# Performance work log

Hardware: AMD Instinct MI355X
Metric: run time of the kernel (lower is better)

The kernel has to match this reference:

```python
import jax, jax.numpy as jnp
import numpy as np

N_HEAD = 16
N_KV_HEAD = 4
D_HEAD = 128
RMS_EPS = 1.1920929e-07  # torch default eps for fp32 rms_norm


def _rms_norm(x):
    return x * jax.lax.rsqrt(jnp.mean(x * x, axis=-1, keepdims=True) + RMS_EPS)


def _rotary_tables(n_pos, dim):
    # dim = d_head; freq table has dim//2 entries (half of them zero)
    angular_freq = (1.0 / 1024.0) ** jnp.linspace(0.0, 1.0, dim // 4, dtype=jnp.float32)
    angular_freq = jnp.concatenate([angular_freq, jnp.zeros(dim // 4, jnp.float32)])
    theta = jnp.arange(n_pos, dtype=jnp.float32)[:, None] * angular_freq[None, :]
    return jnp.cos(theta), jnp.sin(theta)


def _apply_rotary(x):
    # x: (B, H, T, D). Faithful to source: cos/sin indexed by x.shape[-3] (= H),
    # broadcast over the time axis.
    n = x.shape[-3]
    cos, sin = _rotary_tables(n, x.shape[-1])
    cos = cos[None, :, None, :]
    sin = sin[None, :, None, :]
    xf = x.astype(jnp.float32)
    x1, x2 = jnp.split(xf, 2, axis=-1)
    y1 = x1 * cos + x2 * sin
    y2 = -x1 * sin + x2 * cos
    return jnp.concatenate([y1, y2], axis=-1).astype(x.dtype)


def setup_inputs() -> dict:
    key = jax.random.key(0)
    k1, k2, k3, k4 = jax.random.split(key, 4)
    B, T, C = 2, 2048, 2048
    return {
        "x": jax.random.normal(k1, (B, T, C), jnp.float32),
        "Wq": jax.random.normal(k2, (C, C), jnp.float32) * 0.02,
        "Wkv": jax.random.normal(k3, (2 * N_KV_HEAD * D_HEAD, C), jnp.float32) * 0.02,
        "Wproj": jax.random.normal(k4, (C, C), jnp.float32) * 0.02,
        "tok_masks": jnp.ones((B, T), jnp.int32),
    }


def reference(x, Wq, Wkv, Wproj, tok_masks):
    B, T, C = x.shape
    nh, nkv, dh = N_HEAD, N_KV_HEAD, D_HEAD

    q = (x @ Wq.T).reshape(B, T, nh, dh).transpose(0, 2, 1, 3)          # (B,nh,T,dh)
    kv = x @ Wkv.T                                                       # (B,T,2*nkv*dh)
    k, v = jnp.split(kv, 2, axis=2)
    k = k.reshape(B, T, nkv, dh).transpose(0, 2, 1, 3)                   # (B,nkv,T,dh)
    v = v.reshape(B, T, nkv, dh).transpose(0, 2, 1, 3)

    q, k = _rms_norm(q), _rms_norm(k)
    q, k = _apply_rotary(q), _apply_rotary(k)

    # GQA: repeat kv heads to match query heads
    rep = nh // nkv
    k = jnp.repeat(k, rep, axis=1)
    v = jnp.repeat(v, rep, axis=1)

    scale = 1.0 / jnp.sqrt(jnp.float32(dh))
    scores = jnp.einsum("bhqd,bhkd->bhqk", q, k) * scale                 # (B,nh,T,T)
    causal = jnp.tril(jnp.ones((T, T), bool))
    scores = jnp.where(causal[None, None], scores, -jnp.inf)
    attn = jax.nn.softmax(scores, axis=-1)
    y = jnp.einsum("bhqk,bhkd->bhqd", attn, v)                           # (B,nh,T,dh)
    y = y.transpose(0, 2, 1, 3).reshape(B, T, C)
    y = y @ Wproj.T
    return (y, jnp.float32(0.0))
```

## Files before the change

kernel.cpp:

```cpp
#include <hip/hip_runtime.h>
#include <hip/hip_bf16.h>

#define T_SEQ 2048
#define BATCH 2
#define CDIM  2048
#define NH    16
#define NKV   4
#define DH    128

typedef __attribute__((ext_vector_type(8))) short bfrag;
typedef __attribute__((ext_vector_type(4))) float ffrag;
typedef __hip_bfloat16 bf16;

#if defined(__has_builtin)
#if __has_builtin(__builtin_amdgcn_global_load_lds)
#define USE_GLL 1
#endif
#endif
#ifndef USE_GLL
#define USE_GLL 0
#endif

__device__ __forceinline__ void stage16(const bf16* __restrict__ g, bf16* lds_base, int lane) {
#if USE_GLL
    __builtin_amdgcn_global_load_lds((const __attribute__((address_space(1))) void*)g,
                                     (__attribute__((address_space(3))) void*)lds_base, 16, 0, 0);
#else
    *(bfrag*)(lds_base + lane * 8) = *(const bfrag*)g;
#endif
}

struct bf16x4 { bf16 a, b, c, d; };
#define N4_X   (BATCH * T_SEQ * CDIM / 4)
#define N4_WQ  (CDIM * CDIM / 4)
#define N4_WKV (2 * NKV * DH * CDIM / 4)
#define N4_WP  (CDIM * CDIM / 4)
__global__ __launch_bounds__(256) void cast_all(
    const float* __restrict__ x, const float* __restrict__ wq,
    const float* __restrict__ wkv, const float* __restrict__ wp,
    bf16* __restrict__ xb, bf16* __restrict__ wqb, bf16* __restrict__ wkvb, bf16* __restrict__ wpb)
{
    int j = blockIdx.x * 256 + threadIdx.x;
    const float* s; bf16* d;
    if (j < N4_X) { s = x; d = xb; }
    else {
        j -= N4_X;
        if (j < N4_WQ) { s = wq; d = wqb; }
        else {
            j -= N4_WQ;
            if (j < N4_WKV) { s = wkv; d = wkvb; }
            else { j -= N4_WKV; if (j >= N4_WP) return; s = wp; d = wpb; }
        }
    }
    float4 f = ((const float4*)s)[j];
    bf16x4 o{__float2bfloat16(f.x), __float2bfloat16(f.y),
             __float2bfloat16(f.z), __float2bfloat16(f.w)};
    ((bf16x4*)d)[j] = o;
}

template<int MODE>
__device__ __forceinline__ void gemm_body(
    const bf16* __restrict__ A, const bf16* __restrict__ W, int m0, int n0,
    bf16* __restrict__ out0, bf16* __restrict__ out1, float* __restrict__ outf)
{
    __shared__ __align__(16) bf16 sA[128 * 32];
    __shared__ __align__(16) bf16 sB[128 * 32];
    const int lane = threadIdx.x & 63;
    const int w = threadIdx.x >> 6;
    const int lr = lane & 15, quad = lane >> 4;
    const int m_off = (w & 1) * 64, n_off = (w >> 1) * 64;

    const int srow = lane >> 2;
    const int ssw  = (srow + (srow >> 2)) & 3;
    const bf16* ap = A + (size_t)(m0 + w * 32 + srow) * CDIM + (((lane & 3) ^ ssw)) * 8;
    const bf16* bp = W + (size_t)(n0 + w * 32 + srow) * CDIM + (((lane & 3) ^ ssw)) * 8;
    bf16* sA0 = &sA[(w * 32) * 32];
    bf16* sA1 = &sA[(w * 32 + 16) * 32];
    bf16* sB0 = &sB[(w * 32) * 32];
    bf16* sB1 = &sB[(w * 32 + 16) * 32];

    const int rsw = (lr + (lr >> 2)) & 3;
    const int ccol = ((quad ^ rsw)) * 8;

    ffrag acc[4][4] = {};
    for (int kk = 0; kk < CDIM; kk += 32) {
        __syncthreads();
        stage16(ap, sA0, lane);
        stage16(ap + (size_t)16 * CDIM, sA1, lane);
        stage16(bp, sB0, lane);
        stage16(bp + (size_t)16 * CDIM, sB1, lane);
        ap += 32; bp += 32;
        __syncthreads();

        bfrag af[4], bg[4];
        #pragma unroll
        for (int s = 0; s < 4; ++s) af[s] = *(const bfrag*)&sA[(m_off + s * 16 + lr) * 32 + ccol];
        #pragma unroll
        for (int s = 0; s < 4; ++s) bg[s] = *(const bfrag*)&sB[(n_off + s * 16 + lr) * 32 + ccol];
        #pragma unroll
        for (int i = 0; i < 4; ++i)
            #pragma unroll
            for (int j = 0; j < 4; ++j)
                acc[i][j] = __builtin_amdgcn_mfma_f32_16x16x32_bf16(af[i], bg[j], acc[i][j], 0, 0, 0);
    }

    #pragma unroll
    for (int si = 0; si < 4; ++si) {
        #pragma unroll
        for (int sj = 0; sj < 4; ++sj) {
            #pragma unroll
            for (int i = 0; i < 4; ++i) {
                int m = m0 + m_off + si * 16 + quad * 4 + i;
                int n = n0 + n_off + sj * 16 + lr;
                float v = acc[si][sj][i];
                if (MODE == 0) {
                    int b = m >> 11, t = m & (T_SEQ - 1);
                    int h = n >> 7, d = n & (DH - 1);
                    out0[(((size_t)(b * NH + h) * T_SEQ + t) << 7) + d] = __float2bfloat16(v);
                } else if (MODE == 1) {
                    int b = m >> 11, t = m & (T_SEQ - 1);
                    if (n < NKV * DH) {
                        int h = n >> 7, d = n & (DH - 1);
                        out0[(((size_t)(b * NKV + h) * T_SEQ + t) << 7) + d] = __float2bfloat16(v);
                    } else {
                        int n2 = n - NKV * DH;
                        int h = n2 >> 7, d = n2 & (DH - 1);
                        out1[(((size_t)(b * NKV + h) * DH + d) << 11) + t] = __float2bfloat16(v);
                    }
                } else {
                    outf[(size_t)m * CDIM + n] = v;
                }
            }
        }
    }
}

__global__ __launch_bounds__(256) void gemm_qkv(
    const bf16* __restrict__ A, const bf16* __restrict__ Wq, const bf16* __restrict__ Wkv,
    bf16* __restrict__ q, bf16* __restrict__ k, bf16* __restrict__ vt)
{
    if (blockIdx.y < 16)
        gemm_body<0>(A, Wq, blockIdx.x * 128, blockIdx.y * 128, q, nullptr, nullptr);
    else
        gemm_body<1>(A, Wkv, blockIdx.x * 128, (blockIdx.y - 16) * 128, k, vt, nullptr);
}

__global__ __launch_bounds__(256) void gemm_proj(
    const bf16* __restrict__ A, const bf16* __restrict__ W, float* __restrict__ outf)
{
    gemm_body<2>(A, W, blockIdx.x * 128, blockIdx.y * 128, nullptr, nullptr, outf);
    if (blockIdx.x == 0 && blockIdx.y == 0 && threadIdx.x == 0)
        outf[(size_t)BATCH * T_SEQ * CDIM] = 0.0f;
}

#define QROWS (BATCH * NH * T_SEQ)
#define KROWS (BATCH * NKV * T_SEQ)
__global__ __launch_bounds__(256) void normrope_k(bf16* __restrict__ qb, bf16* __restrict__ kb) {
    int row = blockIdx.x * 4 + (threadIdx.x >> 6);
    bf16* bufb; int nheads;
    if (row < QROWS) { bufb = qb; nheads = NH; }
    else { row -= QROWS; bufb = kb; nheads = NKV; }
    const int h = (row >> 11) % nheads;
    bf16* p = bufb + (size_t)row * DH;
    const int d = threadIdx.x & 63;
    float x1 = __bfloat162float(p[d]);
    float x2 = __bfloat162float(p[d + 64]);
    float ss = x1 * x1 + x2 * x2;
    #pragma unroll
    for (int off = 32; off; off >>= 1) ss += __shfl_xor(ss, off);
    float r = rsqrtf(ss * (1.0f / 128.0f) + 1.1920929e-07f);
    x1 *= r; x2 *= r;
    float freq = (d < 32) ? exp2f(-10.0f * (float)d * (1.0f / 31.0f)) : 0.0f;
    float th = (float)h * freq;
    float c, s;
    __sincosf(th, &s, &c);
    p[d]      = __float2bfloat16(x1 * c + x2 * s);
    p[d + 64] = __float2bfloat16(-x1 * s + x2 * c);
}

__global__ __launch_bounds__(512, 2) void attn_k(const bf16* __restrict__ Q, const bf16* __restrict__ K,
                                                 const bf16* __restrict__ VT, bf16* __restrict__ Y)
{
    const int lane = threadIdx.x & 63;
    const int w = threadIdx.x >> 6;
    const int g = w >> 2, wl = w & 3;
    const int p = blockIdx.x, h = blockIdx.y, b = blockIdx.z;
    const int lr = lane & 15, quad = lane >> 4, lk = quad * 8;
    const bf16* Qb = Q  + (size_t)(b * NH  + h)        * T_SEQ * DH;
    const bf16* Kb = K  + (size_t)(b * NKV + (h >> 2)) * T_SEQ * DH;
    const bf16* Vb = VT + (size_t)(b * NKV + (h >> 2)) * DH * T_SEQ;

    __shared__ __align__(16) union ShmU {
        struct { bf16 SK[2][32 * 128]; bf16 SV[2][128 * 32]; bf16 SP[8][2][16 * 32]; } s;
        ffrag MRG[9 * 4 * 64];
    } shm;
    bf16* SKg = shm.s.SK[g];
    bf16* SVg = shm.s.SV[g];

    const int k_r0 = wl * 8 + (lane >> 4);
    const int k_ch = lane & 15;
    const int v_r0 = wl * 32 + (lane >> 2);
    const int v_ch = lane & 3;
    const int vsw = (lr + (lr >> 2)) & 3;
    const int prow_r = ((lr & 3) << 2) | (lr >> 2);
    const int psw = (prow_r + (prow_r >> 2)) & 3;
    const float scale = 0.08838834764831845f;

    for (int pass = 0; pass < 2; ++pass) {
        const int qb = pass ? (15 - p) : p;
        const int nc = 2 * (qb + 1);
        const int q0 = qb * 128 + wl * 32;

        bfrag qf[2][4];
        #pragma unroll
        for (int t = 0; t < 2; ++t)
            #pragma unroll
            for (int dc = 0; dc < 4; ++dc)
                qf[t][dc] = *(const bfrag*)(Qb + (size_t)(q0 + t * 16 + lr) * DH + dc * 32 + lk);

        float lp[2][4] = {};
        ffrag o[2][8] = {};

        bfrag kr[2], vr[2];
        {
            const int b0 = g * 32;
            #pragma unroll
            for (int j = 0; j < 2; ++j) {
                kr[j] = *(const bfrag*)(Kb + (size_t)(b0 + k_r0 + j * 4) * DH + k_ch * 8);
                vr[j] = *(const bfrag*)(Vb + (size_t)(v_r0 + j * 16) * T_SEQ + b0 + v_ch * 8);
            }
        }

        for (int c = 0; c < nc; ++c) {
            const int base = c * 64 + g * 32;
            __syncthreads();
            #pragma unroll
            for (int j = 0; j < 2; ++j) {
                int krow = k_r0 + j * 4;
                *(bfrag*)&SKg[krow * 128 + ((k_ch ^ (krow & 15))) * 8] = kr[j];
                int vrow = v_r0 + j * 16;
                *(bfrag*)&SVg[vrow * 32 + ((v_ch ^ ((vrow + (vrow >> 2)) & 3))) * 8] = vr[j];
            }
            if (c + 1 < nc) {
                const int nb = base + 64;
                #pragma unroll
                for (int j = 0; j < 2; ++j) {
                    kr[j] = *(const bfrag*)(Kb + (size_t)(nb + k_r0 + j * 4) * DH + k_ch * 8);
                    vr[j] = *(const bfrag*)(Vb + (size_t)(v_r0 + j * 16) * T_SEQ + nb + v_ch * 8);
                }
            }
            __syncthreads();

            ffrag s2[2][2] = {};
            #pragma unroll
            for (int kt = 0; kt < 2; ++kt)
                #pragma unroll
                for (int dc = 0; dc < 4; ++dc) {
                    bfrag kf = *(const bfrag*)&SKg[(kt * 16 + lr) * 128 + (((dc << 2) | quad) ^ lr) * 8];
                    s2[0][kt] = __builtin_amdgcn_mfma_f32_16x16x32_bf16(qf[0][dc], kf, s2[0][kt], 0, 0, 0);
                    s2[1][kt] = __builtin_amdgcn_mfma_f32_16x16x32_bf16(qf[1][dc], kf, s2[1][kt], 0, 0, 0);
                }

            const bool maskc = (c >= 2 * qb);
            #pragma unroll
            for (int t = 0; t < 2; ++t)
                #pragma unroll
                for (int kt = 0; kt < 2; ++kt) {
                    const int col = base + kt * 16 + lr;
                    #pragma unroll
                    for (int i = 0; i < 4; ++i) {
                        const int row = q0 + t * 16 + quad * 4 + i;
                        float e = (!maskc || col <= row) ? __expf(fmaf(s2[t][kt][i], scale, -16.0f)) : 0.0f;
                        lp[t][i] += e;
                        const int pr = i * 4 + quad;
                        const int pc = (kt * 2 + (lr >> 3)) ^ ((quad + i) & 3);
                        shm.s.SP[w][t][pr * 32 + pc * 8 + (lr & 7)] = __float2bfloat16(e);
                    }
                }

            bfrag pf0 = *(const bfrag*)&shm.s.SP[w][0][prow_r * 32 + ((quad ^ psw)) * 8];
            bfrag pf1 = *(const bfrag*)&shm.s.SP[w][1][prow_r * 32 + ((quad ^ psw)) * 8];
            #pragma unroll
            for (int dt = 0; dt < 8; ++dt) {
                bfrag vf = *(const bfrag*)&SVg[(dt * 16 + lr) * 32 + ((quad ^ vsw)) * 8];
                o[0][dt] = __builtin_amdgcn_mfma_f32_16x16x32_bf16(pf0, vf, o[0][dt], 0, 0, 0);
                o[1][dt] = __builtin_amdgcn_mfma_f32_16x16x32_bf16(pf1, vf, o[1][dt], 0, 0, 0);
            }
        }

        __syncthreads();
        #pragma unroll
        for (int t = 0; t < 2; ++t) {
            if (g == 1) {
                #pragma unroll
                for (int d = 0; d < 8; ++d) shm.MRG[(d * 4 + wl) * 64 + lane] = o[t][d];
                ffrag l4 = {lp[t][0], lp[t][1], lp[t][2], lp[t][3]};
                shm.MRG[(8 * 4 + wl) * 64 + lane] = l4;
            }
            __syncthreads();
            if (g == 0) {
                #pragma unroll
                for (int d = 0; d < 8; ++d) o[t][d] += shm.MRG[(d * 4 + wl) * 64 + lane];
                ffrag l4 = shm.MRG[(8 * 4 + wl) * 64 + lane];
                float inv[4];
                #pragma unroll
                for (int i = 0; i < 4; ++i) {
                    float l = lp[t][i] + l4[i];
                    #pragma unroll
                    for (int off = 1; off < 16; off <<= 1) l += __shfl_xor(l, off);
                    inv[i] = 1.0f / l;
                }
                #pragma unroll
                for (int dt = 0; dt < 8; ++dt)
                    #pragma unroll
                    for (int i = 0; i < 4; ++i) {
                        int row = q0 + t * 16 + quad * 4 + i;
                        Y[((size_t)(b * T_SEQ) + row) * CDIM + h * DH + dt * 16 + lr] =
                            __float2bfloat16(o[t][dt][i] * inv[i]);
                    }
            }
            __syncthreads();
        }
    }
}

extern "C" void kernel_launch(void* const* d_in, const int* in_sizes, int n_in,
                              void* d_out, int out_size, void* d_ws, size_t ws_size,
                              hipStream_t stream) {
    const float* x     = (const float*)d_in[0];
    const float* Wq    = (const float*)d_in[1];
    const float* Wkv   = (const float*)d_in[2];
    const float* Wproj = (const float*)d_in[3];
    float* out = (float*)d_out;

    char* ws = (char*)d_ws;
    size_t off = 0;
    auto alloc = [&](size_t bytes) { void* p = ws + off; off += (bytes + 255) & ~255ULL; return p; };
    bf16* xb   = (bf16*)alloc((size_t)BATCH * T_SEQ * CDIM * 2);
    bf16* wqb  = (bf16*)alloc((size_t)CDIM * CDIM * 2);
    bf16* wkvb = (bf16*)alloc((size_t)2 * NKV * DH * CDIM * 2);
    bf16* wpb  = (bf16*)alloc((size_t)CDIM * CDIM * 2);
    bf16* qb   = (bf16*)alloc((size_t)BATCH * NH * T_SEQ * DH * 2);
    bf16* kb   = (bf16*)alloc((size_t)BATCH * NKV * T_SEQ * DH * 2);
    bf16* vtb  = (bf16*)alloc((size_t)BATCH * NKV * DH * T_SEQ * 2);
    bf16* y1   = (bf16*)alloc((size_t)BATCH * T_SEQ * CDIM * 2);

    const int total4 = N4_X + N4_WQ + N4_WKV + N4_WP;
    cast_all<<<(total4 + 255) / 256, 256, 0, stream>>>(x, Wq, Wkv, Wproj, xb, wqb, wkvb, wpb);

    gemm_qkv<<<dim3(32, 24), 256, 0, stream>>>(xb, wqb, wkvb, qb, kb, vtb);
    normrope_k<<<(QROWS + KROWS) / 4, 256, 0, stream>>>(qb, kb);
    attn_k<<<dim3(8, NH, BATCH), 512, 0, stream>>>(qb, kb, vtb, y1);
    gemm_proj<<<dim3(32, 16), 256, 0, stream>>>(y1, wpb, out);
}
```

Measured before the change: 299.4 us.

## Rewrite QKV and projection GEMMs with double-buffered LDS pipeline and larger tiles

Replaces the 128x128, K=32 single-buffered GEMM with 8-wave blocks using 256x256 (QKV) and 128x256 (proj) tiles, K=64 steps, and double-buffered LDS. Next-tile global_load_lds prefetches are interleaved across MFMA phases, paced by explicit vmcnt waits and raw barriers, with setprio raised around the MFMA runs. Blocks are remapped through a swizzled 1D grid so neighbouring blocks share operand tiles in L2. The larger tiles and deeper pipeline are meant to hide memory latency and cut barrier overhead. In exchange the grid has fewer blocks, LDS use is much larger, and the hand-tuned wait counts must match the issue order exactly.

```diff
diff --git a/kernel.cpp b/kernel.cpp
--- a/kernel.cpp
+++ b/kernel.cpp
@@ -12,23 +12,31 @@
 typedef __attribute__((ext_vector_type(4))) float ffrag;
 typedef __hip_bfloat16 bf16;
 
-#if defined(__has_builtin)
-#if __has_builtin(__builtin_amdgcn_global_load_lds)
-#define USE_GLL 1
-#endif
-#endif
-#ifndef USE_GLL
-#define USE_GLL 0
-#endif
-
-__device__ __forceinline__ void stage16(const bf16* __restrict__ g, bf16* lds_base, int lane) {
-#if USE_GLL
+__device__ __forceinline__ void gll16(const bf16* __restrict__ g, bf16* lds) {
     __builtin_amdgcn_global_load_lds((const __attribute__((address_space(1))) void*)g,
-                                     (__attribute__((address_space(3))) void*)lds_base, 16, 0, 0);
-#else
-    *(bfrag*)(lds_base + lane * 8) = *(const bfrag*)g;
-#endif
-}
+                                     (__attribute__((address_space(3))) void*)lds, 16, 0, 0);
+}
+
+template<int N> __device__ __forceinline__ void vmw() {
+    static_assert(N >= 0 && N <= 6, "vmcnt range");
+    if constexpr      (N == 0) asm volatile("s_waitcnt vmcnt(0)" ::: "memory");
+    else if constexpr (N == 1) asm volatile("s_waitcnt vmcnt(1)" ::: "memory");
+    else if constexpr (N == 2) asm volatile("s_waitcnt vmcnt(2)" ::: "memory");
+    else if constexpr (N == 3) asm volatile("s_waitcnt vmcnt(3)" ::: "memory");
+    else if constexpr (N == 4) asm volatile("s_waitcnt vmcnt(4)" ::: "memory");
+    else if constexpr (N == 5) asm volatile("s_waitcnt vmcnt(5)" ::: "memory");
+    else                       asm volatile("s_waitcnt vmcnt(6)" ::: "memory");
+}
+__device__ __forceinline__ void barx() {
+    asm volatile("" ::: "memory");
+    __builtin_amdgcn_s_barrier();
+    asm volatile("" ::: "memory");
+}
+
+constexpr int sv_c(int P, int L, int LPP, int p) {
+    return p == P - 1 ? L - 5 : (L - 5) + (p + 1) * (LPP - 1);
+}
+constexpr int dv_c(int L, int p) { int r = L - 5 - (p + 1); return r < 0 ? 0 : r; }
 
 struct bf16x4 { bf16 a, b, c, d; };
 #define N4_X   (BATCH * T_SEQ * CDIM / 4)
@@ -58,74 +66,126 @@
     ((bf16x4*)d)[j] = o;
 }
 
-template<int MODE>
-__device__ __forceinline__ void gemm_body(
+template<int BM, int MODE>
+__device__ __forceinline__ void gemm8_body(
     const bf16* __restrict__ A, const bf16* __restrict__ W, int m0, int n0,
-    bf16* __restrict__ out0, bf16* __restrict__ out1, float* __restrict__ outf)
+    bf16* __restrict__ out0, bf16* __restrict__ out1, float* __restrict__ outf,
+    bf16* __restrict__ sA, bf16* __restrict__ sB)
 {
-    __shared__ __align__(16) bf16 sA[128 * 32];
-    __shared__ __align__(16) bf16 sB[128 * 32];
+    constexpr int MREP = BM / 32;
+    constexpr int P    = MREP / 2;
+    constexpr int LA   = BM / 64;
+    constexpr int L    = LA + 4;
+    constexpr int LPP  = L / P;
+    constexpr int NT   = CDIM / 64;
+    constexpr int ASZ  = BM * 64;
+    constexpr int BSZ  = 256 * 64;
+
     const int lane = threadIdx.x & 63;
-    const int w = threadIdx.x >> 6;
-    const int lr = lane & 15, quad = lane >> 4;
-    const int m_off = (w & 1) * 64, n_off = (w >> 1) * 64;
-
-    const int srow = lane >> 2;
-    const int ssw  = (srow + (srow >> 2)) & 3;
-    const bf16* ap = A + (size_t)(m0 + w * 32 + srow) * CDIM + (((lane & 3) ^ ssw)) * 8;
-    const bf16* bp = W + (size_t)(n0 + w * 32 + srow) * CDIM + (((lane & 3) ^ ssw)) * 8;
-    bf16* sA0 = &sA[(w * 32) * 32];
-    bf16* sA1 = &sA[(w * 32 + 16) * 32];
-    bf16* sB0 = &sB[(w * 32) * 32];
-    bf16* sB1 = &sB[(w * 32 + 16) * 32];
-
-    const int rsw = (lr + (lr >> 2)) & 3;
-    const int ccol = ((quad ^ rsw)) * 8;
-
-    ffrag acc[4][4] = {};
-    for (int kk = 0; kk < CDIM; kk += 32) {
-        __syncthreads();
-        stage16(ap, sA0, lane);
-        stage16(ap + (size_t)16 * CDIM, sA1, lane);
-        stage16(bp, sB0, lane);
-        stage16(bp + (size_t)16 * CDIM, sB1, lane);
-        ap += 32; bp += 32;
-        __syncthreads();
-
-        bfrag af[4], bg[4];
+    const int w    = threadIdx.x >> 6;
+    const int wm   = w >> 2, wn = w & 3;
+    const int lr   = lane & 15, quad = lane >> 4;
+    const int srow = lane >> 3;
+    const int scol = ((lane & 7) ^ srow) << 3;
+
+    const bf16* Ag[LA];
+    const bf16* Bg[4];
+    #pragma unroll
+    for (int j = 0; j < LA; ++j) Ag[j] = A + (size_t)(m0 + j * 64 + w * 8 + srow) * CDIM + scol;
+    #pragma unroll
+    for (int j = 0; j < 4; ++j)  Bg[j] = W + (size_t)(n0 + j * 64 + w * 8 + srow) * CDIM + scol;
+
+    ffrag acc[MREP][4] = {};
+
+    #pragma unroll
+    for (int j = 0; j < 4; ++j)  gll16(Bg[j], sB + j * 4096 + w * 512);
+    #pragma unroll
+    for (int j = 0; j < LA; ++j) gll16(Ag[j], sA + j * 4096 + w * 512);
+    vmw<L - 5>();
+    barx();
+
+    for (int t = 0; t < NT; ++t) {
+        const int cur = t & 1;
+        const bool last = (t == NT - 1);
+        const int knext = (t + 1) * 64;
+        bf16* sAc = sA + cur * ASZ;
+        bf16* sBc = sB + cur * BSZ;
+        bf16* sAn = sA + (cur ^ 1) * ASZ;
+        bf16* sBn = sB + (cur ^ 1) * BSZ;
+        bfrag bgr[2][4];
+
+#define PHASE(pp)                                                                          \
+        {                                                                                  \
+            if (pp == 0) {                                                                 \
+                _Pragma("unroll")                                                          \
+                for (int g = 0; g < 4; ++g) {                                              \
+                    const int br = (wn * 64 + g * 16 + lr) * 64;                           \
+                    bgr[0][g] = *(const bfrag*)&sBc[br + ((quad ^ (lr & 7)) << 3)];        \
+                    bgr[1][g] = *(const bfrag*)&sBc[br + (((4 | quad) ^ (lr & 7)) << 3)];  \
+                }                                                                          \
+            }                                                                              \
+            bfrag af0[2], af1[2];                                                          \
+            _Pragma("unroll")                                                              \
+            for (int f2 = 0; f2 < 2; ++f2) {                                               \
+                const int ar = ((2 * pp + f2) * 32 + wm * 16 + lr) * 64;                   \
+                af0[f2] = *(const bfrag*)&sAc[ar + ((quad ^ (lr & 7)) << 3)];              \
+                af1[f2] = *(const bfrag*)&sAc[ar + (((4 | quad) ^ (lr & 7)) << 3)];        \
+            }                                                                              \
+            if (!last) {                                                                   \
+                _Pragma("unroll")                                                          \
+                for (int l = pp * LPP; l < (pp + 1) * LPP; ++l) {                          \
+                    if (l < 4) gll16(Bg[l] + knext, sBn + l * 4096 + w * 512);             \
+                    else       gll16(Ag[l - 4] + knext, sAn + (l - 4) * 4096 + w * 512);   \
+                }                                                                          \
+            }                                                                              \
+            barx();                                                                        \
+            __builtin_amdgcn_s_setprio(1);                                                 \
+            _Pragma("unroll")                                                              \
+            for (int f2 = 0; f2 < 2; ++f2)                                                 \
+                _Pragma("unroll")                                                          \
+                for (int g = 0; g < 4; ++g) {                                              \
+                    acc[2 * pp + f2][g] = __builtin_amdgcn_mfma_f32_16x16x32_bf16(         \
+                        af0[f2], bgr[0][g], acc[2 * pp + f2][g], 0, 0, 0);                 \
+                    acc[2 * pp + f2][g] = __builtin_amdgcn_mfma_f32_16x16x32_bf16(         \
+                        af1[f2], bgr[1][g], acc[2 * pp + f2][g], 0, 0, 0);                 \
+                }                                                                          \
+            __builtin_amdgcn_s_setprio(0);                                                 \
+            if (!last) vmw<sv_c(P, L, LPP, pp)>();                                         \
+            else if (pp != P - 1) vmw<dv_c(L, pp)>();                                      \
+            barx();                                                                        \
+        }
+
+        PHASE(0)
+        PHASE(1)
+        if constexpr (P == 4) {
+            PHASE(2)
+            PHASE(3)
+        }
+#undef PHASE
+    }
+
+    #pragma unroll
+    for (int f = 0; f < MREP; ++f) {
         #pragma unroll
-        for (int s = 0; s < 4; ++s) af[s] = *(const bfrag*)&sA[(m_off + s * 16 + lr) * 32 + ccol];
-        #pragma unroll
-        for (int s = 0; s < 4; ++s) bg[s] = *(const bfrag*)&sB[(n_off + s * 16 + lr) * 32 + ccol];
-        #pragma unroll
-        for (int i = 0; i < 4; ++i)
-            #pragma unroll
-            for (int j = 0; j < 4; ++j)
-                acc[i][j] = __builtin_amdgcn_mfma_f32_16x16x32_bf16(af[i], bg[j], acc[i][j], 0, 0, 0);
-    }
-
-    #pragma unroll
-    for (int si = 0; si < 4; ++si) {
-        #pragma unroll
-        for (int sj = 0; sj < 4; ++sj) {
+        for (int g = 0; g < 4; ++g) {
             #pragma unroll
             for (int i = 0; i < 4; ++i) {
-                int m = m0 + m_off + si * 16 + quad * 4 + i;
-                int n = n0 + n_off + sj * 16 + lr;
-                float v = acc[si][sj][i];
-                if (MODE == 0) {
-                    int b = m >> 11, t = m & (T_SEQ - 1);
+                const int m = m0 + f * 32 + wm * 16 + quad * 4 + i;
+                const int n = n0 + wn * 64 + g * 16 + lr;
+                const float v = acc[f][g][i];
+                if constexpr (MODE == 0) {
+                    int b = m >> 11, tt = m & (T_SEQ - 1);
                     int h = n >> 7, d = n & (DH - 1);
-                    out0[(((size_t)(b * NH + h) * T_SEQ + t) << 7) + d] = __float2bfloat16(v);
-                } else if (MODE == 1) {
-                    int b = m >> 11, t = m & (T_SEQ - 1);
+                    out0[(((size_t)(b * NH + h) * T_SEQ + tt) << 7) + d] = __float2bfloat16(v);
+                } else if constexpr (MODE == 1) {
+                    int b = m >> 11, tt = m & (T_SEQ - 1);
                     if (n < NKV * DH) {
                         int h = n >> 7, d = n & (DH - 1);
-                        out0[(((size_t)(b * NKV + h) * T_SEQ + t) << 7) + d] = __float2bfloat16(v);
+                        out0[(((size_t)(b * NKV + h) * T_SEQ + tt) << 7) + d] = __float2bfloat16(v);
                     } else {
                         int n2 = n - NKV * DH;
                         int h = n2 >> 7, d = n2 & (DH - 1);
-                        out1[(((size_t)(b * NKV + h) * DH + d) << 11) + t] = __float2bfloat16(v);
+                        out1[(((size_t)(b * NKV + h) * DH + d) << 11) + tt] = __float2bfloat16(v);
                     }
                 } else {
                     outf[(size_t)m * CDIM + n] = v;
@@ -135,21 +195,29 @@
     }
 }
 
-__global__ __launch_bounds__(256) void gemm_qkv(
+__global__ __launch_bounds__(512, 2) void gemm_qkv(
     const bf16* __restrict__ A, const bf16* __restrict__ Wq, const bf16* __restrict__ Wkv,
     bf16* __restrict__ q, bf16* __restrict__ k, bf16* __restrict__ vt)
 {
-    if (blockIdx.y < 16)
-        gemm_body<0>(A, Wq, blockIdx.x * 128, blockIdx.y * 128, q, nullptr, nullptr);
-    else
-        gemm_body<1>(A, Wkv, blockIdx.x * 128, (blockIdx.y - 16) * 128, k, vt, nullptr);
-}
-
-__global__ __launch_bounds__(256) void gemm_proj(
+    __shared__ __align__(16) bf16 sA[2 * 256 * 64];
+    __shared__ __align__(16) bf16 sB[2 * 256 * 64];
+    const int bid = blockIdx.x;
+    const int sb = (bid & 7) * 24 + (bid >> 3);
+    const int mt = sb & 15, nt = sb >> 4;
+    if (nt < 8) gemm8_body<256, 0>(A, Wq,  mt * 256, nt * 256,       q, nullptr, nullptr, sA, sB);
+    else        gemm8_body<256, 1>(A, Wkv, mt * 256, (nt - 8) * 256, k, vt,      nullptr, sA, sB);
+}
+
+__global__ __launch_bounds__(512, 2) void gemm_proj(
     const bf16* __restrict__ A, const bf16* __restrict__ W, float* __restrict__ outf)
 {
-    gemm_body<2>(A, W, blockIdx.x * 128, blockIdx.y * 128, nullptr, nullptr, outf);
-    if (blockIdx.x == 0 && blockIdx.y == 0 && threadIdx.x == 0)
+    __shared__ __align__(16) bf16 sA[2 * 128 * 64];
+    __shared__ __align__(16) bf16 sB[2 * 256 * 64];
+    const int bid = blockIdx.x;
+    const int sb = (bid & 7) * 32 + (bid >> 3);
+    const int mt = sb & 31, nt = sb >> 5;
+    gemm8_body<128, 2>(A, W, mt * 128, nt * 256, nullptr, nullptr, outf, sA, sB);
+    if (blockIdx.x == 0 && threadIdx.x == 0)
         outf[(size_t)BATCH * T_SEQ * CDIM] = 0.0f;
 }
 
@@ -348,8 +416,8 @@
     const int total4 = N4_X + N4_WQ + N4_WKV + N4_WP;
     cast_all<<<(total4 + 255) / 256, 256, 0, stream>>>(x, Wq, Wkv, Wproj, xb, wqb, wkvb, wpb);
 
-    gemm_qkv<<<dim3(32, 24), 256, 0, stream>>>(xb, wqb, wkvb, qb, kb, vtb);
+    gemm_qkv<<<dim3(192), 512, 0, stream>>>(xb, wqb, wkvb, qb, kb, vtb);
     normrope_k<<<(QROWS + KROWS) / 4, 256, 0, stream>>>(qb, kb);
     attn_k<<<dim3(8, NH, BATCH), 512, 0, stream>>>(qb, kb, vtb, y1);
-    gemm_proj<<<dim3(32, 16), 256, 0, stream>>>(y1, wpb, out);
-}
+    gemm_proj<<<dim3(256), 512, 0, stream>>>(y1, wpb, out);
+}
```

Result: slower. 305.7 us (+2.1%).
